# Kernel tuning notes

Hardware: AMD Instinct MI355X
Metric: run time of the kernel (lower is better)

## Reference

```python
import jax, jax.numpy as jnp
import numpy as np

TAU = 0.05
MASK_VAL = -1000000000.0
EPS = 1e-12  # torch F.normalize eps


def _l2norm(x):
    n = jnp.linalg.norm(x, axis=-1, keepdims=True)
    return x / jnp.maximum(n, EPS)


def setup_inputs() -> dict:
    key = jax.random.key(0)
    k1, k2 = jax.random.split(key)
    N, D = 16384, 64
    z1 = jax.random.normal(k1, (N, D), dtype=jnp.float32)
    z2 = jax.random.normal(k2, (N, D), dtype=jnp.float32)
    return {"z1": z1, "z2": z2}


def reference(z1, z2):
    # normalize both views
    z1n = _l2norm(z1)
    z2n = _l2norm(z2)
    N = z1n.shape[0]
    # full similarity matrix [N, N]
    sim = jnp.einsum("nd,md->nm", z1n, z2n) / TAU
    pos = jnp.diagonal(sim)  # sim(z1[i], z2[i]) / tau
    # mask the positive position inside the negatives block (as the torch code does)
    eye = jnp.eye(N, dtype=bool)
    neg = jnp.where(eye, MASK_VAL, sim)
    # logits = [pos, masked row]; label = 0 -> CE = logsumexp(logits) - pos
    logits = jnp.concatenate([pos[:, None], neg], axis=1)  # [N, N+1]
    lse = jax.nn.logsumexp(logits, axis=1)
    loss = jnp.sum(lse - pos) / N
    return loss
```

## Files before the change

kernel.cpp:

```cpp
#include <hip/hip_runtime.h>
#include <hip/hip_bf16.h>


typedef __bf16  bf16x8 __attribute__((ext_vector_type(8)));
typedef float   f32x4  __attribute__((ext_vector_type(4)));

#if __has_builtin(__builtin_amdgcn_exp2f)
#define EXP2F(x) __builtin_amdgcn_exp2f(x)
#else
#define EXP2F(x) exp2f(x)
#endif

#define DDIM        64
#define ROWB        128
#define BM          128
#define NWAVES      8
#define WROWS       16
#define CHUNK       64
#define LDS_STRIDE  144
#define CS          8

__global__ __launch_bounds__(256) void norm_cast_kernel(
    const float* __restrict__ z, __hip_bfloat16* __restrict__ out,
    float scale, int nrows)
{
    int row  = (blockIdx.x * 256 + threadIdx.x) >> 6;
    int lane = threadIdx.x & 63;
    if (row >= nrows) return;
    float v  = z[row * DDIM + lane];
    float ss = v * v;
    #pragma unroll
    for (int off = 32; off; off >>= 1) ss += __shfl_xor(ss, off);
    float n = fmaxf(sqrtf(ss), 1e-12f);
    out[row * DDIM + lane] = __float2bfloat16((v / n) * scale);
}

__global__ __launch_bounds__(512) void infonce_main_kernel(
    const __hip_bfloat16* __restrict__ z1s,
    const __hip_bfloat16* __restrict__ z2s,
    float* __restrict__ rowsum,
    float* __restrict__ posv,
    int N)
{
    __shared__ char lds[CHUNK * LDS_STRIDE];

    const int tid  = threadIdx.x;
    const int wave = tid >> 6;
    const int lane = tid & 63;
    const int q    = lane >> 4;
    const int l15  = lane & 15;

    const int r0      = blockIdx.x * BM;
    const int colspan = N / CS;
    const int c0      = blockIdx.y * colspan;
    const int wr      = r0 + wave * WROWS;

    const char* abase = (const char*)z1s + (size_t)(wr + l15) * ROWB + q * 16;
    const bf16x8 a0 = *(const bf16x8*)(abase);
    const bf16x8 a1 = *(const bf16x8*)(abase + 64);

    float s0 = 0.f, s1 = 0.f, s2 = 0.f, s3 = 0.f;

    const int sc = tid >> 3, sp = tid & 7;

    for (int cc = 0; cc < colspan; cc += CHUNK) {
        __syncthreads();
        *(float4*)(lds + sc * LDS_STRIDE + sp * 16) =
            *(const float4*)((const char*)z2s + (size_t)(c0 + cc + sc) * ROWB + sp * 16);
        __syncthreads();

        #pragma unroll
        for (int ct = 0; ct < CHUNK / 16; ++ct) {
            const char* bbase = lds + (ct * 16 + l15) * LDS_STRIDE + q * 16;
            bf16x8 b0 = *(const bf16x8*)(bbase);
            bf16x8 b1 = *(const bf16x8*)(bbase + 64);
            f32x4 acc = {0.f, 0.f, 0.f, 0.f};
            acc = __builtin_amdgcn_mfma_f32_16x16x32_bf16(a0, b0, acc, 0, 0, 0);
            acc = __builtin_amdgcn_mfma_f32_16x16x32_bf16(a1, b1, acc, 0, 0, 0);

            const int cg = c0 + cc + ct * 16;
            if (cg == wr) {
                #pragma unroll
                for (int i = 0; i < 4; ++i)
                    if (l15 == q * 4 + i) posv[wr + q * 4 + i] = acc[i];
            }
            s0 += EXP2F(acc[0]);
            s1 += EXP2F(acc[1]);
            s2 += EXP2F(acc[2]);
            s3 += EXP2F(acc[3]);
        }
    }

    #pragma unroll
    for (int off = 1; off < 16; off <<= 1) {
        s0 += __shfl_xor(s0, off);
        s1 += __shfl_xor(s1, off);
        s2 += __shfl_xor(s2, off);
        s3 += __shfl_xor(s3, off);
    }
    if (l15 == 0) {
        atomicAdd(&rowsum[wr + q * 4 + 0], s0);
        atomicAdd(&rowsum[wr + q * 4 + 1], s1);
        atomicAdd(&rowsum[wr + q * 4 + 2], s2);
        atomicAdd(&rowsum[wr + q * 4 + 3], s3);
    }
}

__global__ __launch_bounds__(256) void finalize_kernel(
    const float* __restrict__ rowsum, const float* __restrict__ posv,
    float* __restrict__ out, float invN)
{
    int i = blockIdx.x * 256 + threadIdx.x;
    float c = 0.69314718055994531f * (log2f(rowsum[i]) - posv[i]) * invN;
    #pragma unroll
    for (int off = 32; off; off >>= 1) c += __shfl_down(c, off);
    if ((threadIdx.x & 63) == 0) atomicAdd(out, c);
}

extern "C" void kernel_launch(void* const* d_in, const int* in_sizes, int n_in,
                              void* d_out, int out_size, void* d_ws, size_t ws_size,
                              hipStream_t stream)
{
    const float* z1 = (const float*)d_in[0];
    const float* z2 = (const float*)d_in[1];
    const int N = in_sizes[0] / DDIM;

    char* ws = (char*)d_ws;
    __hip_bfloat16* z1s = (__hip_bfloat16*)ws;
    __hip_bfloat16* z2s = (__hip_bfloat16*)(ws + (size_t)N * ROWB);
    float* rowsum = (float*)(ws + 2 * (size_t)N * ROWB);
    float* posv   = (float*)(ws + 2 * (size_t)N * ROWB + (size_t)N * 4);

    hipMemsetAsync(rowsum, 0, (size_t)N * sizeof(float), stream);
    hipMemsetAsync(d_out, 0, sizeof(float), stream);

    const float kScale = 28.853900817779268f;
    norm_cast_kernel<<<N / 4, 256, 0, stream>>>(z1, z1s, kScale, N);
    norm_cast_kernel<<<N / 4, 256, 0, stream>>>(z2, z2s, 1.0f, N);

    dim3 grid(N / BM, CS);
    infonce_main_kernel<<<grid, NWAVES * 64, 0, stream>>>(z1s, z2s, rowsum, posv, N);

    finalize_kernel<<<N / 256, 256, 0, stream>>>(rowsum, posv, (float*)d_out, 1.0f / N);
}
```

Before: 121.4 us.

## Retile main kernel for 64 rows per wave with double-buffered LDS and fused launches

Each wave now keeps four 16-row A fragments in registers, so every B tile read from LDS feeds four MFMA pairs instead of one. The z2 chunk is prefetched into a second, pre-swizzled LDS buffer while the current chunk computes, which removes one barrier per iteration. The two normalization launches are merged into one, the memsets and atomics are replaced by per-split partial sums, and a single-block finalize kernel reduces them. The cost is higher register use and a grid of only 64x8 blocks, and EXP2F now goes through exp2f instead of the amdgcn builtin, which may compile to a slower instruction sequence.

```diff
diff --git a/kernel.cpp b/kernel.cpp
--- a/kernel.cpp
+++ b/kernel.cpp
@@ -5,44 +5,43 @@
 typedef __bf16  bf16x8 __attribute__((ext_vector_type(8)));
 typedef float   f32x4  __attribute__((ext_vector_type(4)));
 
-#if __has_builtin(__builtin_amdgcn_exp2f)
-#define EXP2F(x) __builtin_amdgcn_exp2f(x)
-#else
 #define EXP2F(x) exp2f(x)
-#endif
 
-#define DDIM        64
-#define ROWB        128
-#define BM          128
-#define NWAVES      8
-#define WROWS       16
-#define CHUNK       64
-#define LDS_STRIDE  144
-#define CS          8
+#define DDIM   64
+#define ROWB   128
+#define NW     4
+#define WROWS  64
+#define BM     (NW * WROWS)
+#define CHUNK  64
+#define CS     8
+#define TILEB  2048
+#define BUFB   (4 * TILEB)
 
-__global__ __launch_bounds__(256) void norm_cast_kernel(
-    const float* __restrict__ z, __hip_bfloat16* __restrict__ out,
-    float scale, int nrows)
+__global__ __launch_bounds__(256) void norm_both_kernel(
+    const float* __restrict__ z1, const float* __restrict__ z2,
+    __hip_bfloat16* __restrict__ out, float scale1, int N)
 {
-    int row  = (blockIdx.x * 256 + threadIdx.x) >> 6;
+    int gr   = (blockIdx.x * 256 + threadIdx.x) >> 6;
     int lane = threadIdx.x & 63;
-    if (row >= nrows) return;
-    float v  = z[row * DDIM + lane];
+    const float* src = (gr < N) ? (z1 + (size_t)gr * DDIM)
+                                : (z2 + (size_t)(gr - N) * DDIM);
+    float scale = (gr < N) ? scale1 : 1.0f;
+    float v  = src[lane];
     float ss = v * v;
     #pragma unroll
     for (int off = 32; off; off >>= 1) ss += __shfl_xor(ss, off);
     float n = fmaxf(sqrtf(ss), 1e-12f);
-    out[row * DDIM + lane] = __float2bfloat16((v / n) * scale);
+    out[(size_t)gr * DDIM + lane] = __float2bfloat16((v / n) * scale);
 }
 
-__global__ __launch_bounds__(512) void infonce_main_kernel(
+__global__ __launch_bounds__(256) void infonce_main_kernel(
     const __hip_bfloat16* __restrict__ z1s,
     const __hip_bfloat16* __restrict__ z2s,
-    float* __restrict__ rowsum,
+    float* __restrict__ partial,
     float* __restrict__ posv,
     int N)
 {
-    __shared__ char lds[CHUNK * LDS_STRIDE];
+    __shared__ char lds[2 * BUFB];
 
     const int tid  = threadIdx.x;
     const int wave = tid >> 6;
@@ -50,71 +49,117 @@
     const int q    = lane >> 4;
     const int l15  = lane & 15;
 
-    const int r0      = blockIdx.x * BM;
     const int colspan = N / CS;
     const int c0      = blockIdx.y * colspan;
-    const int wr      = r0 + wave * WROWS;
+    const int wr      = blockIdx.x * BM + wave * WROWS;
 
-    const char* abase = (const char*)z1s + (size_t)(wr + l15) * ROWB + q * 16;
-    const bf16x8 a0 = *(const bf16x8*)(abase);
-    const bf16x8 a1 = *(const bf16x8*)(abase + 64);
+    bf16x8 a0[4], a1[4];
+    #pragma unroll
+    for (int s = 0; s < 4; ++s) {
+        const char* ab = (const char*)z1s + (size_t)(wr + s * 16 + l15) * ROWB + q * 16;
+        a0[s] = *(const bf16x8*)(ab);
+        a1[s] = *(const bf16x8*)(ab + 64);
+    }
 
-    float s0 = 0.f, s1 = 0.f, s2 = 0.f, s3 = 0.f;
+    float sum[16];
+    #pragma unroll
+    for (int k = 0; k < 16; ++k) sum[k] = 0.f;
 
-    const int sc = tid >> 3, sp = tid & 7;
+    const int gsA = tid, gsB = tid + 256;
+    const int rowA = ((gsA >> 7) << 4) | (gsA & 15);
+    const int rowB = ((gsB >> 7) << 4) | (gsB & 15);
+    const int pA = (((gsA & 127) >> 6) << 2) | (((gsA & 127) >> 4) & 3);
+    const int pB = (((gsB & 127) >> 6) << 2) | (((gsB & 127) >> 4) & 3);
+    const char* z2b = (const char*)z2s;
 
+    *(float4*)(lds + gsA * 16) = *(const float4*)(z2b + (size_t)(c0 + rowA) * ROWB + pA * 16);
+    *(float4*)(lds + gsB * 16) = *(const float4*)(z2b + (size_t)(c0 + rowB) * ROWB + pB * 16);
+    __syncthreads();
+
+    int pb = 0;
     for (int cc = 0; cc < colspan; cc += CHUNK) {
+        float4 vA, vB;
+        const bool has_next = (cc + CHUNK) < colspan;
+        if (has_next) {
+            const int nc = c0 + cc + CHUNK;
+            vA = *(const float4*)(z2b + (size_t)(nc + rowA) * ROWB + pA * 16);
+            vB = *(const float4*)(z2b + (size_t)(nc + rowB) * ROWB + pB * 16);
+        }
+
+        const char* buf = lds + pb * BUFB;
+        #pragma unroll
+        for (int ct = 0; ct < 4; ++ct) {
+            const char* bb = buf + ct * TILEB + lane * 16;
+            bf16x8 b0 = *(const bf16x8*)(bb);
+            bf16x8 b1 = *(const bf16x8*)(bb + 1024);
+            const int cg = c0 + cc + ct * 16;
+            #pragma unroll
+            for (int s = 0; s < 4; ++s) {
+                f32x4 acc = {0.f, 0.f, 0.f, 0.f};
+                acc = __builtin_amdgcn_mfma_f32_16x16x32_bf16(a0[s], b0, acc, 0, 0, 0);
+                acc = __builtin_amdgcn_mfma_f32_16x16x32_bf16(a1[s], b1, acc, 0, 0, 0);
+                if (cg == wr + s * 16) {
+                    #pragma unroll
+                    for (int i = 0; i < 4; ++i)
+                        if (l15 == q * 4 + i) posv[cg + q * 4 + i] = acc[i];
+                }
+                sum[s * 4 + 0] += EXP2F(acc[0]);
+                sum[s * 4 + 1] += EXP2F(acc[1]);
+                sum[s * 4 + 2] += EXP2F(acc[2]);
+                sum[s * 4 + 3] += EXP2F(acc[3]);
+            }
+        }
+
+        if (has_next) {
+            char* nbuf = lds + (pb ^ 1) * BUFB;
+            *(float4*)(nbuf + gsA * 16) = vA;
+            *(float4*)(nbuf + gsB * 16) = vB;
+        }
         __syncthreads();
-        *(float4*)(lds + sc * LDS_STRIDE + sp * 16) =
-            *(const float4*)((const char*)z2s + (size_t)(c0 + cc + sc) * ROWB + sp * 16);
-        __syncthreads();
-
-        #pragma unroll
-        for (int ct = 0; ct < CHUNK / 16; ++ct) {
-            const char* bbase = lds + (ct * 16 + l15) * LDS_STRIDE + q * 16;
-            bf16x8 b0 = *(const bf16x8*)(bbase);
-            bf16x8 b1 = *(const bf16x8*)(bbase + 64);
-            f32x4 acc = {0.f, 0.f, 0.f, 0.f};
-            acc = __builtin_amdgcn_mfma_f32_16x16x32_bf16(a0, b0, acc, 0, 0, 0);
-            acc = __builtin_amdgcn_mfma_f32_16x16x32_bf16(a1, b1, acc, 0, 0, 0);
-
-            const int cg = c0 + cc + ct * 16;
-            if (cg == wr) {
-                #pragma unroll
-                for (int i = 0; i < 4; ++i)
-                    if (l15 == q * 4 + i) posv[wr + q * 4 + i] = acc[i];
-            }
-            s0 += EXP2F(acc[0]);
-            s1 += EXP2F(acc[1]);
-            s2 += EXP2F(acc[2]);
-            s3 += EXP2F(acc[3]);
-        }
+        pb ^= 1;
     }
 
     #pragma unroll
-    for (int off = 1; off < 16; off <<= 1) {
-        s0 += __shfl_xor(s0, off);
-        s1 += __shfl_xor(s1, off);
-        s2 += __shfl_xor(s2, off);
-        s3 += __shfl_xor(s3, off);
+    for (int k = 0; k < 16; ++k) {
+        float v = sum[k];
+        #pragma unroll
+        for (int off = 1; off < 16; off <<= 1) v += __shfl_xor(v, off);
+        sum[k] = v;
     }
     if (l15 == 0) {
-        atomicAdd(&rowsum[wr + q * 4 + 0], s0);
-        atomicAdd(&rowsum[wr + q * 4 + 1], s1);
-        atomicAdd(&rowsum[wr + q * 4 + 2], s2);
-        atomicAdd(&rowsum[wr + q * 4 + 3], s3);
+        float* dst = partial + (size_t)blockIdx.y * N + wr;
+        #pragma unroll
+        for (int s = 0; s < 4; ++s)
+            #pragma unroll
+            for (int i = 0; i < 4; ++i)
+                dst[s * 16 + q * 4 + i] = sum[s * 4 + i];
     }
 }
 
-__global__ __launch_bounds__(256) void finalize_kernel(
-    const float* __restrict__ rowsum, const float* __restrict__ posv,
-    float* __restrict__ out, float invN)
+__global__ __launch_bounds__(1024) void finalize_kernel(
+    const float* __restrict__ partial, const float* __restrict__ posv,
+    float* __restrict__ out, int N)
 {
-    int i = blockIdx.x * 256 + threadIdx.x;
-    float c = 0.69314718055994531f * (log2f(rowsum[i]) - posv[i]) * invN;
+    __shared__ float red[16];
+    float acc = 0.f;
+    for (int base = 0; base < N; base += 1024) {
+        int row = base + threadIdx.x;
+        float s = 0.f;
+        #pragma unroll
+        for (int c = 0; c < CS; ++c) s += partial[(size_t)c * N + row];
+        acc += log2f(s) - posv[row];
+    }
     #pragma unroll
-    for (int off = 32; off; off >>= 1) c += __shfl_down(c, off);
-    if ((threadIdx.x & 63) == 0) atomicAdd(out, c);
+    for (int off = 32; off; off >>= 1) acc += __shfl_xor(acc, off);
+    int wave = threadIdx.x >> 6, lane = threadIdx.x & 63;
+    if (lane == 0) red[wave] = acc;
+    __syncthreads();
+    if (wave == 0) {
+        float v = (lane < 16) ? red[lane] : 0.f;
+        #pragma unroll
+        for (int off = 8; off; off >>= 1) v += __shfl_xor(v, off);
+        if (lane == 0) *out = 0.69314718055994531f * v / (float)N;
+    }
 }
 
 extern "C" void kernel_launch(void* const* d_in, const int* in_sizes, int n_in,
@@ -127,19 +172,16 @@
 
     char* ws = (char*)d_ws;
     __hip_bfloat16* z1s = (__hip_bfloat16*)ws;
-    __hip_bfloat16* z2s = (__hip_bfloat16*)(ws + (size_t)N * ROWB);
-    float* rowsum = (float*)(ws + 2 * (size_t)N * ROWB);
-    float* posv   = (float*)(ws + 2 * (size_t)N * ROWB + (size_t)N * 4);
-
-    hipMemsetAsync(rowsum, 0, (size_t)N * sizeof(float), stream);
-    hipMemsetAsync(d_out, 0, sizeof(float), stream);
+    __hip_bfloat16* z2s = z1s + (size_t)N * DDIM;
+    float* partial = (float*)(ws + 2 * (size_t)N * ROWB);
+    float* posv    = partial + (size_t)CS * N;
 
     const float kScale = 28.853900817779268f;
-    norm_cast_kernel<<<N / 4, 256, 0, stream>>>(z1, z1s, kScale, N);
-    norm_cast_kernel<<<N / 4, 256, 0, stream>>>(z2, z2s, 1.0f, N);
+
+    norm_both_kernel<<<2 * N / 4, 256, 0, stream>>>(z1, z2, z1s, kScale, N);
 
     dim3 grid(N / BM, CS);
-    infonce_main_kernel<<<grid, NWAVES * 64, 0, stream>>>(z1s, z2s, rowsum, posv, N);
+    infonce_main_kernel<<<grid, NW * 64, 0, stream>>>(z1s, z2s, partial, posv, N);
 
-    finalize_kernel<<<N / 256, 256, 0, stream>>>(rowsum, posv, (float*)d_out, 1.0f / N);
+    finalize_kernel<<<1, 1024, 0, stream>>>(partial, posv, (float*)d_out, N);
 }
```

Result: slower. 161.1 us (+32.7%).
